# Kernel tuning notes

Measured on AMD Instinct MI355X. Metric: run time of the kernel, lower is better.

Reference implementation:

```python
import jax, jax.numpy as jnp
import numpy as np

N, E, G = 50000, 320000, 256
BN_EPS = 1e-5
HEADS = 4


def _bn(x, g, b):
    # eval-mode BatchNorm1d with running_mean=0, running_var=1
    return g * (x * np.float32(1.0 / np.sqrt(1.0 + BN_EPS))) + b


def _mlp(x, w1, b1, w2, b2):
    return jax.nn.relu(x @ w1 + b1) @ w2 + b2


def _gatv2(x, src, dst, ea, lw, lb, rw, rb, ew, att, bias):
    n = x.shape[0]
    H = HEADS
    C = lw.shape[1] // H
    # self-loops with edge_attr = mean of incoming edge features (fill_value='mean')
    deg = jax.ops.segment_sum(jnp.ones((ea.shape[0],), x.dtype), dst, num_segments=n)
    loop_ea = jax.ops.segment_sum(ea, dst, num_segments=n) / jnp.maximum(deg, 1.0)[:, None]
    ar = jnp.arange(n)
    s = jnp.concatenate([src, ar])
    d = jnp.concatenate([dst, ar])
    ea_all = jnp.concatenate([ea, loop_ea], axis=0)
    xl = (x @ lw + lb).reshape(n, H, C)   # lin_l (source / message features)
    xr = (x @ rw + rb).reshape(n, H, C)   # lin_r (target)
    ee = (ea_all @ ew).reshape(-1, H, C)  # lin_edge (no bias)
    m = jax.nn.leaky_relu(xl[s] + xr[d] + ee, 0.2)       # [E+N, H, C]
    a = jnp.einsum('ehc,hc->eh', m, att)                 # attention logits
    amax = jax.ops.segment_max(a, d, num_segments=n)
    ex = jnp.exp(a - amax[d])
    den = jax.ops.segment_sum(ex, d, num_segments=n)
    w = ex / den[d]                                      # scatter-softmax over target
    out = jax.ops.segment_sum(xl[s] * w[..., None], d, num_segments=n)
    return out.reshape(n, H * C) + bias


def _meta(x, ea, u, src, dst, batch, ep, gp, up):
    # EdgeModel -> NodeModel(GATv2 + relu) -> GlobalModel (residuals=False, eval dropout)
    ea2 = _mlp(jnp.concatenate([x[src], x[dst], ea], axis=1), *ep)
    xn = jax.nn.relu(_gatv2(x, src, dst, ea2, *gp))
    pooled = jax.ops.segment_sum(xn, batch, num_segments=G)
    u2 = _mlp(jnp.concatenate([u, pooled], axis=1), *up)
    return xn, ea2, u2


def _forward(x, edge_attr, e1_w1, e1_b1, e1_w2, e1_b2, g1_lw, g1_lb, g1_rw, g1_rb, g1_ew, g1_att, g1_bias, u1_w1, u1_b1, u1_w2, u1_b2, bn_n_g, bn_n_b, bn_e_g, bn_e_b, bn_u_g, bn_u_b, e2_w1, e2_b1, e2_w2, e2_b2, g2_lw, g2_lb, g2_rw, g2_rb, g2_ew, g2_att, g2_bias, u2_w1, u2_b1, u2_w2, u2_b2, fc1_w, fc1_b, fc2_w, fc2_b, src, dst, batch):
    u0 = jnp.zeros((G, 256), x.dtype)
    x1, ea1, u1 = _meta(x, edge_attr, u0, src, dst, batch,
                        (e1_w1, e1_b1, e1_w2, e1_b2),
                        (g1_lw, g1_lb, g1_rw, g1_rb, g1_ew, g1_att, g1_bias),
                        (u1_w1, u1_b1, u1_w2, u1_b2))
    x1 = _bn(x1, bn_n_g, bn_n_b)
    ea1 = _bn(ea1, bn_e_g, bn_e_b)
    u1 = _bn(u1, bn_u_g, bn_u_b)
    _, _, u2 = _meta(x1, ea1, u1, src, dst, batch,
                     (e2_w1, e2_b1, e2_w2, e2_b2),
                     (g2_lw, g2_lb, g2_rw, g2_rb, g2_ew, g2_att, g2_bias),
                     (u2_w1, u2_b1, u2_w2, u2_b2))
    h = jax.nn.relu(u2 @ fc1_w + fc1_b)
    return h @ fc2_w + fc2_b


def setup_inputs() -> dict:
    key = jax.random.key(0)
    ks = iter(jax.random.split(key, 64))
    rp = lambda shape: jax.random.normal(next(ks), shape, jnp.float32) * 0.05
    inp = {}
    inp['x'] = jax.random.normal(next(ks), (N, 64), jnp.float32)
    inp['edge_attr'] = jax.random.normal(next(ks), (E, 16), jnp.float32)
    # layer 1: EdgeModel(64,16,h=64,out=128), GATv2(64->256,H=4,edge=128), Global(256+256->256)
    inp.update(e1_w1=rp((144, 64)), e1_b1=rp((64,)), e1_w2=rp((64, 128)), e1_b2=rp((128,)))
    inp.update(g1_lw=rp((64, 256)), g1_lb=rp((256,)), g1_rw=rp((64, 256)), g1_rb=rp((256,)),
               g1_ew=rp((128, 256)), g1_att=rp((4, 64)), g1_bias=rp((256,)))
    inp.update(u1_w1=rp((512, 256)), u1_b1=rp((256,)), u1_w2=rp((256, 256)), u1_b2=rp((256,)))
    inp.update(bn_n_g=jnp.ones((256,), jnp.float32), bn_n_b=jnp.zeros((256,), jnp.float32),
               bn_e_g=jnp.ones((128,), jnp.float32), bn_e_b=jnp.zeros((128,), jnp.float32),
               bn_u_g=jnp.ones((256,), jnp.float32), bn_u_b=jnp.zeros((256,), jnp.float32))
    # layer 2: EdgeModel(256,128,h=128,out=128), GATv2(256->256,H=4,edge=128), Global
    inp.update(e2_w1=rp((640, 128)), e2_b1=rp((128,)), e2_w2=rp((128, 128)), e2_b2=rp((128,)))
    inp.update(g2_lw=rp((256, 256)), g2_lb=rp((256,)), g2_rw=rp((256, 256)), g2_rb=rp((256,)),
               g2_ew=rp((128, 256)), g2_att=rp((4, 64)), g2_bias=rp((256,)))
    inp.update(u2_w1=rp((512, 256)), u2_b1=rp((256,)), u2_w2=rp((256, 256)), u2_b2=rp((256,)))
    inp.update(fc1_w=rp((256, 64)), fc1_b=rp((64,)), fc2_w=rp((64, 1)), fc2_b=rp((1,)))
    inp['edge_index'] = jax.random.randint(next(ks), (2, E), 0, N, jnp.int64)
    inp['batch'] = jnp.sort(jax.random.randint(next(ks), (N,), 0, G, jnp.int64))
    return inp


def reference(x, edge_attr, e1_w1, e1_b1, e1_w2, e1_b2, g1_lw, g1_lb, g1_rw, g1_rb, g1_ew, g1_att, g1_bias, u1_w1, u1_b1, u1_w2, u1_b2, bn_n_g, bn_n_b, bn_e_g, bn_e_b, bn_u_g, bn_u_b, e2_w1, e2_b1, e2_w2, e2_b2, g2_lw, g2_lb, g2_rw, g2_rb, g2_ew, g2_att, g2_bias, u2_w1, u2_b1, u2_w2, u2_b2, fc1_w, fc1_b, fc2_w, fc2_b, edge_index, batch):
    return _forward(x, edge_attr, e1_w1, e1_b1, e1_w2, e1_b2, g1_lw, g1_lb, g1_rw, g1_rb, g1_ew, g1_att, g1_bias, u1_w1, u1_b1, u1_w2, u1_b2, bn_n_g, bn_n_b, bn_e_g, bn_e_b, bn_u_g, bn_u_b, e2_w1, e2_b1, e2_w2, e2_b2, g2_lw, g2_lb, g2_rw, g2_rb, g2_ew, g2_att, g2_bias, u2_w1, u2_b1, u2_w2, u2_b2, fc1_w, fc1_b, fc2_w, fc2_b, edge_index[0], edge_index[1], batch)
```

## Files before the change

### kernel.cpp

```cpp
#include <hip/hip_runtime.h>
#include <hip/hip_bf16.h>
#include <hip/hip_fp8.h>
#include <cstdint>
#include <cstddef>

#define INVS 0.99999500003749968f
#define G_GRAPHS 256

using bf16 = __hip_bfloat16;
using short8 = __attribute__((ext_vector_type(8))) short;
using floatx4 = __attribute__((ext_vector_type(4))) float;

__device__ __forceinline__ unsigned short f2bf(float v) {
    union { float f; unsigned u; } x; x.f = v;
    unsigned r = x.u + 0x7fffu + ((x.u >> 16) & 1u);
    return (unsigned short)(r >> 16);
}
__device__ __forceinline__ float bfu(unsigned short u) { return __uint_as_float((unsigned)u << 16); }
__device__ __forceinline__ unsigned char f2fp8(float v) {
    __hip_fp8_e4m3 q(v); return q.__x;
}
__device__ __forceinline__ float fp82f(unsigned char b) {
    __hip_fp8_e4m3 q; q.__x = b; return (float)q;
}

__global__ void degi_k(const int* __restrict__ dst, int* __restrict__ degi, int E) {
    int gid = blockIdx.x * 256 + threadIdx.x;
    if (gid < E) atomicAdd(&degi[dst[gid]], 1);
}

__global__ __launch_bounds__(1024) void scan_blk_k(const int* __restrict__ degi,
                                                   int* __restrict__ off,
                                                   int* __restrict__ bsum, int N) {
    __shared__ int buf[1024];
    int t = threadIdx.x;
    int base = blockIdx.x * 2048;
    int i0 = base + 2 * t, i1 = base + 2 * t + 1;
    int v0 = (i0 < N) ? (degi[i0] + 1) : 0;
    int v1 = (i1 < N) ? (degi[i1] + 1) : 0;
    int s = v0 + v1;
    buf[t] = s;
    __syncthreads();
    for (int ofs = 1; ofs < 1024; ofs <<= 1) {
        int add = (t >= ofs) ? buf[t - ofs] : 0;
        __syncthreads();
        buf[t] += add;
        __syncthreads();
    }
    int excl = buf[t] - s;
    if (i0 < N) off[i0] = excl;
    if (i1 < N) off[i1] = excl + v0;
    if (t == 1023) bsum[blockIdx.x] = buf[1023];
}

__global__ void scan_top_k(const int* __restrict__ bsum, int* __restrict__ boff,
                           int* __restrict__ off, int NBLK, int N) {
    if (threadIdx.x == 0 && blockIdx.x == 0) {
        int run = 0;
        for (int i = 0; i < NBLK; ++i) { boff[i] = run; run += bsum[i]; }
        off[N] = run;
    }
}

__global__ void scan_add_k(int* __restrict__ off, const int* __restrict__ boff, int N) {
    int gid = blockIdx.x * 256 + threadIdx.x;
    if (gid < N) off[gid] += boff[gid >> 11];
}

__global__ void fill_csr_k(const int* __restrict__ src, const int* __restrict__ dst,
                           const int* __restrict__ off, int* __restrict__ fillc,
                           int* __restrict__ csr_src, int* __restrict__ csr_dst,
                           int* __restrict__ csr_eid, int E, int N) {
    int gid = blockIdx.x * 256 + threadIdx.x;
    if (gid < E) {
        int d = dst[gid];
        int slot = off[d] + atomicAdd(&fillc[d], 1);
        csr_src[slot] = src[gid];
        csr_dst[slot] = d;
        csr_eid[slot] = gid;
    }
    if (gid < N) {
        int slot = off[gid + 1] - 1;
        csr_src[slot] = gid;
        csr_dst[slot] = gid;
        csr_eid[slot] = E + gid;
    }
}

__global__ void conv_weights1_k(const float* __restrict__ w1, const float* __restrict__ w2,
                                short* __restrict__ w1p, short* __restrict__ w1c,
                                short* __restrict__ w2s) {
    int gid = blockIdx.x * 256 + threadIdx.x;
    if (gid < 1024) {
        int f = gid >> 6, lane = gid & 63;
        int kk = f >> 3, tt = f & 7;
        int n = tt * 16 + (lane & 15);
        int k0 = kk * 32 + (lane >> 4) * 8;
        short8 v;
        for (int j = 0; j < 8; ++j) {
            int k = k0 + j;
            float x = (n < 64) ? w1[k * 64 + n] : w1[(64 + k) * 64 + (n - 64)];
            v[j] = (short)f2bf(x);
        }
        *(short8*)(w1p + (long long)gid * 8) = v;
    } else if (gid < 1280) {
        int g2 = gid - 1024;
        int tt = g2 >> 6, lane = g2 & 63;
        int n = tt * 16 + (lane & 15);
        int k0 = (lane >> 4) * 8;
        short8 v;
        for (int j = 0; j < 8; ++j) {
            int k = k0 + j;
            v[j] = (k < 16) ? (short)f2bf(w1[(128 + k) * 64 + n]) : (short)0;
        }
        *(short8*)(w1c + (long long)g2 * 8) = v;
    } else if (gid < 2304) {
        int g2 = gid - 1280;
        int f = g2 >> 6, lane = g2 & 63;
        int kk = f >> 3, tt = f & 7;
        int n = tt * 16 + (lane & 15);
        int k0 = kk * 32 + (lane >> 4) * 8;
        short8 v;
        for (int j = 0; j < 8; ++j) v[j] = (short)f2bf(w2[(k0 + j) * 128 + n]);
        *(short8*)(w2s + (long long)g2 * 8) = v;
    }
}

__global__ void conv_ew_k(const float* __restrict__ ew, short* __restrict__ ews) {
    int gid = blockIdx.x * 256 + threadIdx.x;
    if (gid >= 4096) return;
    int f = gid >> 6, lane = gid & 63;
    int kk = f >> 4, tt = f & 15;
    int n = tt * 16 + (lane & 15);
    int k0 = kk * 32 + (lane >> 4) * 8;
    short8 v;
    for (int j = 0; j < 8; ++j) v[j] = (short)f2bf(ew[(k0 + j) * 256 + n]);
    *(short8*)(ews + (long long)gid * 8) = v;
}

template <int K>
__global__ void conv_nodew_k(const float* __restrict__ wl, const float* __restrict__ wr,
                             short* __restrict__ out) {
    int gid = blockIdx.x * 256 + threadIdx.x;
    if (gid >= (K / 32) * 32 * 64) return;
    int f = gid >> 6, lane = gid & 63;
    int kk = f >> 5, tt = f & 31;
    int n = tt * 16 + (lane & 15);
    int k0 = kk * 32 + (lane >> 4) * 8;
    short8 v;
    for (int j = 0; j < 8; ++j) {
        int k = k0 + j;
        float x = (n < 256) ? wl[k * 256 + n] : wr[k * 256 + (n - 256)];
        v[j] = (short)f2bf(x);
    }
    *(short8*)(out + (long long)gid * 8) = v;
}

__global__ void conv_pre2w_k(const float* __restrict__ w1, short* __restrict__ out) {
    int gid = blockIdx.x * 256 + threadIdx.x;
    if (gid >= 8 * 16 * 64) return;
    int f = gid >> 6, lane = gid & 63;
    int kk = f >> 4, tt = f & 15;
    int n = tt * 16 + (lane & 15);
    int k0 = kk * 32 + (lane >> 4) * 8;
    short8 v;
    for (int j = 0; j < 8; ++j) {
        int k = k0 + j;
        float x = (n < 128) ? w1[k * 128 + n] : w1[(256 + k) * 128 + (n - 128)];
        v[j] = (short)f2bf(x);
    }
    *(short8*)(out + (long long)gid * 8) = v;
}

__global__ __launch_bounds__(256) void pre1_mfma_k(
    const float* __restrict__ x, const short* __restrict__ w1p,
    const float* __restrict__ b1, bf16* __restrict__ pre1, int N) {
    __shared__ short At[16][72];
    __shared__ short Ot[16][136];
    int t = threadIdx.x;
    long long n0 = (long long)blockIdx.x * 16;
    {
        int r = t >> 4, c = t & 15;
        long long n = n0 + r;
        float4 v = {0.f, 0.f, 0.f, 0.f};
        if (n < N) v = *(const float4*)(x + n * 64 + c * 4);
        ushort4 pk;
        pk.x = f2bf(v.x); pk.y = f2bf(v.y); pk.z = f2bf(v.z); pk.w = f2bf(v.w);
        *(ushort4*)&At[r][c * 4] = pk;
    }
    __syncthreads();
    int w = t >> 6, lane = t & 63;
    int nq = w * 2;
    int lr = lane & 15, lq = lane >> 4;
    floatx4 acc[2];
    for (int i = 0; i < 2; ++i) acc[i] = (floatx4){0.f, 0.f, 0.f, 0.f};
    for (int kk = 0; kk < 2; ++kk) {
        short8 a = *(const short8*)&At[lr][kk * 32 + lq * 8];
        for (int tt = 0; tt < 2; ++tt) {
            short8 b = *(const short8*)(w1p + ((long long)((kk * 8 + nq + tt) * 64 + lane)) * 8);
            acc[tt] = __builtin_amdgcn_mfma_f32_16x16x32_bf16(a, b, acc[tt], 0, 0, 0);
        }
    }
    for (int tt = 0; tt < 2; ++tt) {
        int col = (nq + tt) * 16 + lr;
        float bv = (col >= 64) ? b1[col - 64] : 0.f;
        for (int r = 0; r < 4; ++r)
            Ot[lq * 4 + r][col] = (short)f2bf(acc[tt][r] + bv);
    }
    __syncthreads();
    {
        int r = t >> 4, c = t & 15;
        long long n = n0 + r;
        if (n < N)
            *(short8*)(void*)(pre1 + n * 128 + c * 8) = *(const short8*)&Ot[r][c * 8];
    }
}

__global__ __launch_bounds__(256) void edge_mlp1_mfma_k(
    const bf16* __restrict__ pre1, const float* __restrict__ ea,
    const int* __restrict__ csr_src, const int* __restrict__ csr_dst,
    const int* __restrict__ csr_eid,
    const short* __restrict__ w1c,
    const short* __restrict__ w2s, const float* __restrict__ b2,
    const short* __restrict__ ews,
    bf16* __restrict__ out, unsigned char* __restrict__ ee8, int NT, int E) {
    __shared__ float Ps[32][68];
    __shared__ short Ae[32][40];
    __shared__ short Ht[32][72];
    __shared__ short A2[32][136];
    __shared__ int sdv[32][3];
    unsigned char* Et = (unsigned char*)&Ps[0][0];
    int t = threadIdx.x;
    long long s0 = (long long)blockIdx.x * 32;
    if (t < 96) {
        int r = t & 31, which = t >> 5;
        long long s = s0 + r;
        int v = (which == 2) ? E : 0;
        if (s < NT) v = (which == 0) ? csr_src[s] : (which == 1 ? csr_dst[s] : csr_eid[s]);
        sdv[r][which] = v;
    }
    __syncthreads();
    {
        int r = t >> 3, c = t & 7;
        long long s = s0 + r;
        bool ok = (s < NT) && (sdv[r][2] < E);
        float p[8];
        if (ok) {
            short8 vs = *(const short8*)(const void*)(pre1 + (long long)sdv[r][0] * 128 + c * 8);
            short8 vd = *(const short8*)(const void*)(pre1 + (long long)sdv[r][1] * 128 + 64 + c * 8);
            for (int j = 0; j < 8; ++j)
                p[j] = bfu((unsigned short)vs[j]) + bfu((unsigned short)vd[j]);
        } else {
            for (int j = 0; j < 8; ++j) p[j] = 0.f;
        }
        for (int j = 0; j < 8; ++j) Ps[r][c * 8 + j] = p[j];
    }
    if (t < 128) {
        int r = t >> 2, c = t & 3;
        long long s = s0 + r;
        int eid = sdv[r][2];
        float4 v = {0.f, 0.f, 0.f, 0.f};
        if (s < NT && eid < E) v = *(const float4*)(ea + (long long)eid * 16 + c * 4);
        ushort4 pk;
        pk.x = f2bf(v.x); pk.y = f2bf(v.y); pk.z = f2bf(v.z); pk.w = f2bf(v.w);
        *(ushort4*)&Ae[r][c * 4] = pk;
    } else {
        int i = t - 128;
        int r = i >> 2, c = i & 3;
        *(ushort4*)&Ae[r][16 + c * 4] = (ushort4){0, 0, 0, 0};
    }
    __syncthreads();

    int w = t >> 6, lane = t & 63;
    int m0 = (w & 1) * 16;
    int lr = lane & 15, lq = lane >> 4;

    {
        int nq1 = (w >> 1) * 2;
        floatx4 acc[2];
        for (int tt = 0; tt < 2; ++tt) {
            int col = (nq1 + tt) * 16 + lr;
            for (int r = 0; r < 4; ++r) acc[tt][r] = Ps[m0 + lq * 4 + r][col];
        }
        short8 a = *(const short8*)&Ae[m0 + lr][lq * 8];
        for (int tt = 0; tt < 2; ++tt) {
            short8 b = *(const short8*)(w1c + ((long long)((nq1 + tt) * 64 + lane)) * 8);
            acc[tt] = __builtin_amdgcn_mfma_f32_16x16x32_bf16(a, b, acc[tt], 0, 0, 0);
        }
        for (int tt = 0; tt < 2; ++tt) {
            int col = (nq1 + tt) * 16 + lr;
            for (int r = 0; r < 4; ++r)
                Ht[m0 + lq * 4 + r][col] = (short)f2bf(fmaxf(acc[tt][r], 0.f));
        }
    }
    __syncthreads();

    {
        int nq2 = (w >> 1) * 4;
        floatx4 acc2[4];
        for (int i = 0; i < 4; ++i) acc2[i] = (floatx4){0.f, 0.f, 0.f, 0.f};
        for (int kk = 0; kk < 2; ++kk) {
            short8 a = *(const short8*)&Ht[m0 + lr][kk * 32 + lq * 8];
            for (int tt = 0; tt < 4; ++tt) {
                short8 b = *(const short8*)(w2s + ((long long)((kk * 8 + nq2 + tt) * 64 + lane)) * 8);
                acc2[tt] = __builtin_amdgcn_mfma_f32_16x16x32_bf16(a, b, acc2[tt], 0, 0, 0);
            }
        }
        for (int tt = 0; tt < 4; ++tt) {
            int col = (nq2 + tt) * 16 + lr;
            float bv = b2[col];
            for (int r = 0; r < 4; ++r)
                A2[m0 + lq * 4 + r][col] = (short)f2bf(acc2[tt][r] + bv);
        }
    }
    __syncthreads();

    {
        int nq3 = (w >> 1) * 8;
        floatx4 acc3[8];
        for (int i = 0; i < 8; ++i) acc3[i] = (floatx4){0.f, 0.f, 0.f, 0.f};
        for (int kk = 0; kk < 4; ++kk) {
            short8 a = *(const short8*)&A2[m0 + lr][kk * 32 + lq * 8];
            for (int tt = 0; tt < 8; ++tt) {
                short8 b = *(const short8*)(ews + ((long long)((kk * 16 + nq3 + tt) * 64 + lane)) * 8);
                acc3[tt] = __builtin_amdgcn_mfma_f32_16x16x32_bf16(a, b, acc3[tt], 0, 0, 0);
            }
        }
        for (int tt = 0; tt < 8; ++tt) {
            int col = (nq3 + tt) * 16 + lr;
            for (int r = 0; r < 4; ++r)
                Et[(m0 + lq * 4 + r) * 272 + col] = f2fp8(acc3[tt][r]);
        }
    }
    for (int i = t; i < 512; i += 256) {
        int r = i >> 4, c = i & 15;
        long long s = s0 + r;
        if (s < NT)
            *(short8*)(void*)(out + s * 128 + c * 8) = *(const short8*)&A2[r][c * 8];
    }
    __syncthreads();
    for (int i = t; i < 512; i += 256) {
        int r = i >> 4, c = i & 15;
        long long s = s0 + r;
        if (s < NT)
            *(uint4*)(ee8 + s * 256 + c * 16) = *(const uint4*)(Et + r * 272 + c * 16);
    }
}

template <int K, typename T>
__global__ __launch_bounds__(256) void node_linear_mfma_k(
    const T* x, const short* __restrict__ ws,
    const float* __restrict__ bl, const float* __restrict__ br,
    bf16* __restrict__ xl, bf16* xr, int N) {
    __shared__ short At[16][K + 8];
    __shared__ short Ot[16][520];
    int t = threadIdx.x;
    long long n0 = (long long)blockIdx.x * 16;
    if (sizeof(T) == 4) {
        for (int i = t; i < 16 * (K / 4); i += 256) {
            int r = i / (K / 4), c = i % (K / 4);
            long long n = n0 + r;
            float4 v = {0.f, 0.f, 0.f, 0.f};
            if (n < N) v = *(const float4*)((const float*)x + n * K + c * 4);
            ushort4 pk;
            pk.x = f2bf(v.x); pk.y = f2bf(v.y); pk.z = f2bf(v.z); pk.w = f2bf(v.w);
            *(ushort4*)&At[r][c * 4] = pk;
        }
    } else {
        for (int i = t; i < 16 * (K / 8); i += 256) {
            int r = i / (K / 8), c = i % (K / 8);
            long long n = n0 + r;
            short8 v = {0, 0, 0, 0, 0, 0, 0, 0};
            if (n < N) v = *(const short8*)(const void*)((const bf16*)x + n * K + c * 8);
            *(short8*)&At[r][c * 8] = v;
        }
    }
    __syncthreads();

    int w = t >> 6, lane = t & 63;
    int nq = w * 8;
    int lr = lane & 15, lq = lane >> 4;

    floatx4 acc[8];
    for (int i = 0; i < 8; ++i) acc[i] = (floatx4){0.f, 0.f, 0.f, 0.f};
    for (int kk = 0; kk < K / 32; ++kk) {
        short8 a = *(const short8*)&At[lr][kk * 32 + lq * 8];
        for (int tt = 0; tt < 8; ++tt) {
            short8 b = *(const short8*)(ws + ((long long)((kk * 32 + nq + tt) * 64 + lane)) * 8);
            acc[tt] = __builtin_amdgcn_mfma_f32_16x16x32_bf16(a, b, acc[tt], 0, 0, 0);
        }
    }
    for (int tt = 0; tt < 8; ++tt) {
        int col = (nq + tt) * 16 + lr;
        float bv = (col < 256) ? bl[col] : br[col - 256];
        for (int r = 0; r < 4; ++r)
            Ot[lq * 4 + r][col] = (short)f2bf(acc[tt][r] + bv);
    }
    __syncthreads();
    for (int i = t; i < 1024; i += 256) {
        int r = i >> 6, c = i & 63;
        long long n = n0 + r;
        if (n < N) {
            short8 v = *(const short8*)&Ot[r][c * 8];
            if (c < 32) *(short8*)(void*)(xl + n * 256 + c * 8) = v;
            else        *(short8*)(void*)(xr + n * 256 + (c - 32) * 8) = v;
        }
    }
}

__global__ __launch_bounds__(256) void pre_mfma_k(
    const bf16* __restrict__ x, const short* __restrict__ ws,
    const float* __restrict__ bx, bf16* __restrict__ out, int N) {
    __shared__ short At[16][264];
    __shared__ short Ot[16][264];
    int t = threadIdx.x;
    long long n0 = (long long)blockIdx.x * 16;
    for (int i = t; i < 512; i += 256) {
        int r = i >> 5, c = i & 31;
        long long n = n0 + r;
        short8 v = {0, 0, 0, 0, 0, 0, 0, 0};
        if (n < N) v = *(const short8*)(const void*)(x + n * 256 + c * 8);
        *(short8*)&At[r][c * 8] = v;
    }
    __syncthreads();

    int w = t >> 6, lane = t & 63;
    int nq = w * 4;
    int lr = lane & 15, lq = lane >> 4;

    floatx4 acc[4];
    for (int i = 0; i < 4; ++i) acc[i] = (floatx4){0.f, 0.f, 0.f, 0.f};
    for (int kk = 0; kk < 8; ++kk) {
        short8 a = *(const short8*)&At[lr][kk * 32 + lq * 8];
        for (int tt = 0; tt < 4; ++tt) {
            short8 b = *(const short8*)(ws + ((long long)((kk * 16 + nq + tt) * 64 + lane)) * 8);
            acc[tt] = __builtin_amdgcn_mfma_f32_16x16x32_bf16(a, b, acc[tt], 0, 0, 0);
        }
    }
    for (int tt = 0; tt < 4; ++tt) {
        int col = (nq + tt) * 16 + lr;
        float bv = bx[col];
        for (int r = 0; r < 4; ++r)
            Ot[lq * 4 + r][col] = (short)f2bf(acc[tt][r] + bv);
    }
    __syncthreads();
    for (int i = t; i < 512; i += 256) {
        int r = i >> 5, c = i & 31;
        long long n = n0 + r;
        if (n < N)
            *(short8*)(void*)(out + n * 256 + c * 8) = *(const short8*)&Ot[r][c * 8];
    }
}

template <bool L1>
__global__ __launch_bounds__(256) void gat_fused_k(
    const unsigned char* __restrict__ ee8, const bf16* __restrict__ xl, const bf16* xr,
    const int* __restrict__ off, const int* __restrict__ csr_src,
    const float* __restrict__ att, const float* __restrict__ bias,
    const float* __restrict__ bng, const float* __restrict__ bnb,
    const int* __restrict__ batch,
    bf16* x1bn, float* __restrict__ pooled, int N) {
    __shared__ float ps[4][260];
    __shared__ int bid[4];
    int t = threadIdx.x;
    int w = t >> 6, lane = t & 63;
    int n = blockIdx.x * 4 + w;
    bool valid = n < N;
    int c0 = lane * 4;
    float o0 = 0.f, o1 = 0.f, o2 = 0.f, o3 = 0.f;
    if (valid) {
        ushort4 xrp = *(const ushort4*)(const void*)(xr + (long long)n * 256 + c0);
        ushort4 xop = *(const ushort4*)(const void*)(xl + (long long)n * 256 + c0);
        float xr0 = bfu(xrp.x), xr1 = bfu(xrp.y), xr2 = bfu(xrp.z), xr3 = bfu(xrp.w);
        float4 atv = *(const float4*)(att + c0);
        float a0 = 0.f, a1 = 0.f, a2 = 0.f, a3 = 0.f, dacc = 0.f;
        float es0 = 0.f, es1 = 0.f, es2 = 0.f, es3 = 0.f;
        int beg = off[n], end1 = off[n + 1] - 1;
        ushort4 xlp;
        unsigned ep;
        {
            int sid = csr_src[beg];
            xlp = *(const ushort4*)(const void*)(xl + (long long)sid * 256 + c0);
            ep = *(const unsigned*)(ee8 + (long long)beg * 256 + c0);
        }
        for (int i = beg; i < end1; ++i) {
            ushort4 cx = xlp;
            unsigned ce = ep;
            if (i + 1 < end1) {
                int sid = csr_src[i + 1];
                xlp = *(const ushort4*)(const void*)(xl + (long long)sid * 256 + c0);
                ep = *(const unsigned*)(ee8 + (long long)(i + 1) * 256 + c0);
            }
            float x0 = bfu(cx.x), x1 = bfu(cx.y), x2 = bfu(cx.z), x3 = bfu(cx.w);
            float e0 = fp82f(ce & 0xff);
            float e1 = fp82f((ce >> 8) & 0xff);
            float e2 = fp82f((ce >> 16) & 0xff);
            float e3 = fp82f(ce >> 24);
            es0 += e0; es1 += e1; es2 += e2; es3 += e3;
            float m0 = x0 + xr0 + e0;
            float m1 = x1 + xr1 + e1;
            float m2 = x2 + xr2 + e2;
            float m3 = x3 + xr3 + e3;
            m0 = m0 > 0.f ? m0 : 0.2f * m0;
            m1 = m1 > 0.f ? m1 : 0.2f * m1;
            m2 = m2 > 0.f ? m2 : 0.2f * m2;
            m3 = m3 > 0.f ? m3 : 0.2f * m3;
            float p = atv.x * m0 + atv.y * m1 + atv.z * m2 + atv.w * m3;
            p += __shfl_xor(p, 1, 64);
            p += __shfl_xor(p, 2, 64);
            p += __shfl_xor(p, 4, 64);
            p += __shfl_xor(p, 8, 64);
            float ex = expf(p);
            a0 += ex * x0; a1 += ex * x1; a2 += ex * x2; a3 += ex * x3;
            dacc += ex;
        }
        {
            float rdv = 1.f / fmaxf((float)(end1 - beg), 1.f);
            float x0 = bfu(xop.x), x1 = bfu(xop.y), x2 = bfu(xop.z), x3 = bfu(xop.w);
            float m0 = x0 + xr0 + es0 * rdv;
            float m1 = x1 + xr1 + es1 * rdv;
            float m2 = x2 + xr2 + es2 * rdv;
            float m3 = x3 + xr3 + es3 * rdv;
            m0 = m0 > 0.f ? m0 : 0.2f * m0;
            m1 = m1 > 0.f ? m1 : 0.2f * m1;
            m2 = m2 > 0.f ? m2 : 0.2f * m2;
            m3 = m3 > 0.f ? m3 : 0.2f * m3;
            float p = atv.x * m0 + atv.y * m1 + atv.z * m2 + atv.w * m3;
            p += __shfl_xor(p, 1, 64);
            p += __shfl_xor(p, 2, 64);
            p += __shfl_xor(p, 4, 64);
            p += __shfl_xor(p, 8, 64);
            float ex = expf(p);
            a0 += ex * x0; a1 += ex * x1; a2 += ex * x2; a3 += ex * x3;
            dacc += ex;
        }
        float inv = 1.f / dacc;
        o0 = fmaxf(a0 * inv + bias[c0],     0.f);
        o1 = fmaxf(a1 * inv + bias[c0 + 1], 0.f);
        o2 = fmaxf(a2 * inv + bias[c0 + 2], 0.f);
        o3 = fmaxf(a3 * inv + bias[c0 + 3], 0.f);
        if (L1) {
            ushort4 o;
            o.x = f2bf(bng[c0]     * (o0 * INVS) + bnb[c0]);
            o.y = f2bf(bng[c0 + 1] * (o1 * INVS) + bnb[c0 + 1]);
            o.z = f2bf(bng[c0 + 2] * (o2 * INVS) + bnb[c0 + 2]);
            o.w = f2bf(bng[c0 + 3] * (o3 * INVS) + bnb[c0 + 3]);
            *(ushort4*)(void*)(x1bn + (long long)n * 256 + c0) = o;
        }
    }
    if (lane == 0) bid[w] = valid ? batch[n] : -1;
    ps[w][c0]     = o0;
    ps[w][c0 + 1] = o1;
    ps[w][c0 + 2] = o2;
    ps[w][c0 + 3] = o3;
    __syncthreads();
    int b0 = bid[0];
    bool same = (b0 >= 0)
             && (bid[1] < 0 || bid[1] == b0)
             && (bid[2] < 0 || bid[2] == b0)
             && (bid[3] < 0 || bid[3] == b0);
    if (same) {
        float s = ps[0][t] + ps[1][t] + ps[2][t] + ps[3][t];
        atomicAdd(&pooled[(long long)b0 * 256 + t], s);
    } else if (valid) {
        long long pb = (long long)bid[w] * 256 + c0;
        atomicAdd(&pooled[pb],     o0);
        atomicAdd(&pooled[pb + 1], o1);
        atomicAdd(&pooled[pb + 2], o2);
        atomicAdd(&pooled[pb + 3], o3);
    }
}

__global__ void global_mlp1_k(const float* __restrict__ pooled,
                              const float* __restrict__ w1, const float* __restrict__ b1,
                              const float* __restrict__ w2, const float* __restrict__ b2,
                              const float* __restrict__ bng, const float* __restrict__ bnb,
                              float* __restrict__ u1bn) {
    __shared__ float pr[256];
    __shared__ float h[256];
    int t = threadIdx.x, g = blockIdx.x;
    pr[t] = pooled[g * 256 + t];
    __syncthreads();
    float acc = b1[t];
    for (int k = 0; k < 256; ++k) acc += pr[k] * w1[(256 + k) * 256 + t];
    h[t] = fmaxf(acc, 0.f);
    __syncthreads();
    float a2 = b2[t];
    for (int k = 0; k < 256; ++k) a2 += h[k] * w2[k * 256 + t];
    u1bn[g * 256 + t] = bng[t] * (a2 * INVS) + bnb[t];
}

__global__ void conv_weights_k(const float* __restrict__ w1, const float* __restrict__ w2,
                               const float* __restrict__ b1,
                               const float* __restrict__ bg, const float* __restrict__ bb,
                               short* __restrict__ w1s, short* __restrict__ w2s,
                               float* __restrict__ b1x) {
    int gid = blockIdx.x * 256 + threadIdx.x;
    if (gid < 10240) {
        int f = gid >> 6, lane = gid & 63;
        int kk = f >> 3, tt = f & 7;
        int n = tt * 16 + (lane & 15);
        int k0 = kk * 32 + (lane >> 4) * 8;
        short8 v;
        for (int j = 0; j < 8; ++j) {
            int k = k0 + j;
            float x = w1[k * 128 + n];
            if (k >= 512) x *= bg[k - 512] * INVS;
            v[j] = (short)f2bf(x);
        }
        *(short8*)(w1s + (long long)gid * 8) = v;
    } else if (gid < 12288) {
        int g2 = gid - 10240;
        int f = g2 >> 6, lane = g2 & 63;
        int kk = f >> 3, tt = f & 7;
        int n = tt * 16 + (lane & 15);
        int k0 = kk * 32 + (lane >> 4) * 8;
        short8 v;
        for (int j = 0; j < 8; ++j) v[j] = (short)f2bf(w2[(k0 + j) * 128 + n]);
        *(short8*)(w2s + (long long)g2 * 8) = v;
    } else if (gid < 12544) {
        int j = gid - 12288;
        b1x[j] = 0.f;
    } else if (gid < 12672) {
        int j = gid - 12544;
        float acc = b1[j];
        for (int c = 0; c < 128; ++c) acc += bb[c] * w1[(512 + c) * 128 + j];
        b1x[128 + j] = acc;
    }
}

__global__ __launch_bounds__(256) void edge_mlp2_mfma_k(
    const bf16* __restrict__ xpre, const bf16* __restrict__ ea_slot,
    const int* __restrict__ csr_src, const int* __restrict__ csr_dst,
    const int* __restrict__ csr_eid,
    const short* __restrict__ w1s,
    const short* __restrict__ w2s, const float* __restrict__ b2,
    const short* __restrict__ ews,
    unsigned char* __restrict__ ee8, int NT, int E) {
    __shared__ float Ps[32][132];
    __shared__ short At[32][136];
    __shared__ short Ht[32][136];
    __shared__ int sdv[32][3];
    unsigned char* Et = (unsigned char*)&Ps[0][0];
    int t = threadIdx.x;
    long long s0 = (long long)blockIdx.x * 32;
    if (t < 96) {
        int r = t & 31, which = t >> 5;
        long long s = s0 + r;
        int v = (which == 2) ? E : 0;
        if (s < NT) v = (which == 0) ? csr_src[s] : (which == 1 ? csr_dst[s] : csr_eid[s]);
        sdv[r][which] = v;
    }
    __syncthreads();
    for (int i = t; i < 512; i += 256) {
        int r = i >> 4, c = i & 15;
        long long s = s0 + r;
        bool ok = (s < NT) && (sdv[r][2] < E);
        float p[8];
        if (ok) {
            short8 vs = *(const short8*)(const void*)(xpre + (long long)sdv[r][0] * 256 + c * 8);
            short8 vd = *(const short8*)(const void*)(xpre + (long long)sdv[r][1] * 256 + 128 + c * 8);
            for (int j = 0; j < 8; ++j)
                p[j] = bfu((unsigned short)vs[j]) + bfu((unsigned short)vd[j]);
        } else {
            for (int j = 0; j < 8; ++j) p[j] = 0.f;
        }
        for (int j = 0; j < 8; ++j) Ps[r][c * 8 + j] = p[j];
    }
    for (int i = t; i < 512; i += 256) {
        int r = i >> 4, c = i & 15;
        long long s = s0 + r;
        short8 v = {0, 0, 0, 0, 0, 0, 0, 0};
        if (s < NT && sdv[r][2] < E)
            v = *(const short8*)(const void*)(ea_slot + s * 128 + c * 8);
        *(short8*)&At[r][c * 8] = v;
    }
    __syncthreads();

    int w = t >> 6, lane = t & 63;
    int m0 = (w & 1) * 16;
    int nq = (w >> 1) * 4;
    int lr = lane & 15, lq = lane >> 4;

    floatx4 acc[4];
    for (int tt = 0; tt < 4; ++tt) {
        int col = (nq + tt) * 16 + lr;
        for (int r = 0; r < 4; ++r) acc[tt][r] = Ps[m0 + lq * 4 + r][col];
    }
    for (int kk = 0; kk < 4; ++kk) {
        short8 a = *(const short8*)&At[m0 + lr][kk * 32 + lq * 8];
        for (int tt = 0; tt < 4; ++tt) {
            short8 b = *(const short8*)(w1s + ((long long)(((16 + kk) * 8 + nq + tt) * 64 + lane)) * 8);
            acc[tt] = __builtin_amdgcn_mfma_f32_16x16x32_bf16(a, b, acc[tt], 0, 0, 0);
        }
    }
    for (int tt = 0; tt < 4; ++tt) {
        int col = (nq + tt) * 16 + lr;
        for (int r = 0; r < 4; ++r)
            Ht[m0 + lq * 4 + r][col] = (short)f2bf(fmaxf(acc[tt][r], 0.f));
    }
    __syncthreads();

    floatx4 acc2[4];
    for (int i = 0; i < 4; ++i) acc2[i] = (floatx4){0.f, 0.f, 0.f, 0.f};
    for (int kk = 0; kk < 4; ++kk) {
        short8 a = *(const short8*)&Ht[m0 + lr][kk * 32 + lq * 8];
        for (int tt = 0; tt < 4; ++tt) {
            short8 b = *(const short8*)(w2s + ((long long)((kk * 8 + nq + tt) * 64 + lane)) * 8);
            acc2[tt] = __builtin_amdgcn_mfma_f32_16x16x32_bf16(a, b, acc2[tt], 0, 0, 0);
        }
    }
    for (int tt = 0; tt < 4; ++tt) {
        int col = (nq + tt) * 16 + lr;
        float bv = b2[col];
        for (int r = 0; r < 4; ++r)
            At[m0 + lq * 4 + r][col] = (short)f2bf(acc2[tt][r] + bv);
    }
    __syncthreads();
    {
        int nq3 = (w >> 1) * 8;
        floatx4 acc3[8];
        for (int i = 0; i < 8; ++i) acc3[i] = (floatx4){0.f, 0.f, 0.f, 0.f};
        for (int kk = 0; kk < 4; ++kk) {
            short8 a = *(const short8*)&At[m0 + lr][kk * 32 + lq * 8];
            for (int tt = 0; tt < 8; ++tt) {
                short8 b = *(const short8*)(ews + ((long long)((kk * 16 + nq3 + tt) * 64 + lane)) * 8);
                acc3[tt] = __builtin_amdgcn_mfma_f32_16x16x32_bf16(a, b, acc3[tt], 0, 0, 0);
            }
        }
        for (int tt = 0; tt < 8; ++tt) {
            int col = (nq3 + tt) * 16 + lr;
            for (int r = 0; r < 4; ++r)
                Et[(m0 + lq * 4 + r) * 272 + col] = f2fp8(acc3[tt][r]);
        }
    }
    __syncthreads();
    for (int i = t; i < 512; i += 256) {
        int r = i >> 4, c = i & 15;
        long long s = s0 + r;
        if (s < NT && sdv[r][2] < E)
            *(uint4*)(ee8 + s * 256 + c * 16) = *(const uint4*)(Et + r * 272 + c * 16);
    }
}

__global__ void final_mlp_k(const float* __restrict__ u1bn, const float* __restrict__ pooled,
                            const float* __restrict__ w1, const float* __restrict__ b1,
                            const float* __restrict__ w2, const float* __restrict__ b2,
                            const float* __restrict__ f1w, const float* __restrict__ f1b,
                            const float* __restrict__ f2w, const float* __restrict__ f2b,
                            float* __restrict__ out) {
    __shared__ float ub[256], pb[256], h[256], u2[256];
    int t = threadIdx.x, g = blockIdx.x;
    ub[t] = u1bn[g * 256 + t];
    pb[t] = pooled[g * 256 + t];
    __syncthreads();
    float acc = b1[t];
    for (int k = 0; k < 256; ++k)
        acc += ub[k] * w1[k * 256 + t] + pb[k] * w1[(256 + k) * 256 + t];
    h[t] = fmaxf(acc, 0.f);
    __syncthreads();
    float a2 = b2[t];
    for (int k = 0; k < 256; ++k) a2 += h[k] * w2[k * 256 + t];
    u2[t] = a2;
    __syncthreads();
    float fv = 0.f;
    if (t < 64) {
        float a3 = f1b[t];
        for (int k = 0; k < 256; ++k) a3 += u2[k] * f1w[k * 64 + t];
        fv = fmaxf(a3, 0.f) * f2w[t];
    }
    for (int off = 32; off; off >>= 1) fv += __shfl_down(fv, off, 64);
    if (t == 0) out[g] = fv + f2b[0];
}

extern "C" void kernel_launch(void* const* d_in, const int* in_sizes, int n_in,
                              void* d_out, int out_size, void* d_ws, size_t ws_size,
                              hipStream_t stream) {
    const float* x         = (const float*)d_in[0];
    const float* edge_attr = (const float*)d_in[1];
    const float* e1_w1 = (const float*)d_in[2];
    const float* e1_b1 = (const float*)d_in[3];
    const float* e1_w2 = (const float*)d_in[4];
    const float* e1_b2 = (const float*)d_in[5];
    const float* g1_lw = (const float*)d_in[6];
    const float* g1_lb = (const float*)d_in[7];
    const float* g1_rw = (const float*)d_in[8];
    const float* g1_rb = (const float*)d_in[9];
    const float* g1_ew = (const float*)d_in[10];
    const float* g1_att = (const float*)d_in[11];
    const float* g1_bias = (const float*)d_in[12];
    const float* u1_w1 = (const float*)d_in[13];
    const float* u1_b1 = (const float*)d_in[14];
    const float* u1_w2 = (const float*)d_in[15];
    const float* u1_b2 = (const float*)d_in[16];
    const float* bn_n_g = (const float*)d_in[17];
    const float* bn_n_b = (const float*)d_in[18];
    const float* bn_e_g = (const float*)d_in[19];
    const float* bn_e_b = (const float*)d_in[20];
    const float* bn_u_g = (const float*)d_in[21];
    const float* bn_u_b = (const float*)d_in[22];
    const float* e2_w1 = (const float*)d_in[23];
    const float* e2_b1 = (const float*)d_in[24];
    const float* e2_w2 = (const float*)d_in[25];
    const float* e2_b2 = (const float*)d_in[26];
    const float* g2_lw = (const float*)d_in[27];
    const float* g2_lb = (const float*)d_in[28];
    const float* g2_rw = (const float*)d_in[29];
    const float* g2_rb = (const float*)d_in[30];
    const float* g2_ew = (const float*)d_in[31];
    const float* g2_att = (const float*)d_in[32];
    const float* g2_bias = (const float*)d_in[33];
    const float* u2_w1 = (const float*)d_in[34];
    const float* u2_b1 = (const float*)d_in[35];
    const float* u2_w2 = (const float*)d_in[36];
    const float* u2_b2 = (const float*)d_in[37];
    const float* fc1_w = (const float*)d_in[38];
    const float* fc1_b = (const float*)d_in[39];
    const float* fc2_w = (const float*)d_in[40];
    const float* fc2_b = (const float*)d_in[41];
    const int* edge_index = (const int*)d_in[42];
    const int* batch = (const int*)d_in[43];

    const int N = in_sizes[0] / 64;
    const int E = in_sizes[1] / 16;
    const int NT = E + N;
    const int G = G_GRAPHS;
    const int* src = edge_index;
    const int* dst = edge_index + E;
    const int NB = (NT + 31) / 32;
    const int NSB = (N + 2047) / 2048;

    char* p = (char*)d_ws;
    auto alloc = [&](size_t bytes) { char* r = p; p += (bytes + 255) & ~(size_t)255; return r; };
    bf16* eabuf = (bf16*)alloc((size_t)NT * 128 * 2);
    bf16* xl    = (bf16*)alloc((size_t)N * 256 * 2);
    bf16* xr    = (bf16*)alloc((size_t)N * 256 * 2);
    bf16* x1bn  = xr;
    unsigned char* ee8 = (unsigned char*)alloc((size_t)NT * 256);
    bf16* pre1  = (bf16*)alloc((size_t)N * 128 * 2);
    int* degi   = (int*)alloc((size_t)N * 4);
    int* off    = (int*)alloc((size_t)(N + 1) * 4);
    int* fillc  = (int*)alloc((size_t)N * 4);
    int* csr_src = (int*)alloc((size_t)NT * 4);
    int* csr_dst = (int*)alloc((size_t)NT * 4);
    int* csr_eid = (int*)alloc((size_t)NT * 4);
    int* bsum   = (int*)alloc((size_t)(NSB + 1) * 4);
    int* boff   = (int*)alloc((size_t)(NSB + 1) * 4);
    float* pooled = (float*)alloc((size_t)G * 256 * 4);
    float* u1bn = (float*)alloc((size_t)G * 256 * 4);
    short* w1s  = (short*)alloc((size_t)20 * 8 * 64 * 8 * 2);
    short* w2s  = (short*)alloc((size_t)4 * 8 * 64 * 8 * 2);
    float* b1x  = (float*)alloc((size_t)256 * 4);
    short* w1p  = (short*)alloc((size_t)16 * 64 * 8 * 2);
    short* w1c  = (short*)alloc((size_t)4 * 64 * 8 * 2);
    short* w2s1 = (short*)alloc((size_t)16 * 64 * 8 * 2);
    short* ews1 = (short*)alloc((size_t)4 * 16 * 64 * 8 * 2);
    short* ews2 = (short*)alloc((size_t)4 * 16 * 64 * 8 * 2);
    short* nw1  = (short*)alloc((size_t)2 * 32 * 64 * 8 * 2);
    short* nw2  = (short*)alloc((size_t)8 * 32 * 64 * 8 * 2);
    short* nwp  = (short*)alloc((size_t)8 * 16 * 64 * 8 * 2);

    hipMemsetAsync(degi, 0, (size_t)N * 4, stream);
    hipMemsetAsync(fillc, 0, (size_t)N * 4, stream);
    hipMemsetAsync(pooled, 0, (size_t)G * 256 * 4, stream);
    degi_k<<<(E + 255) / 256, 256, 0, stream>>>(dst, degi, E);
    scan_blk_k<<<NSB, 1024, 0, stream>>>(degi, off, bsum, N);
    scan_top_k<<<1, 64, 0, stream>>>(bsum, boff, off, NSB, N);
    scan_add_k<<<(N + 255) / 256, 256, 0, stream>>>(off, boff, N);
    fill_csr_k<<<(max(E, N) + 255) / 256, 256, 0, stream>>>(src, dst, off, fillc,
                                                            csr_src, csr_dst, csr_eid, E, N);

    conv_weights1_k<<<9, 256, 0, stream>>>(e1_w1, e1_w2, w1p, w1c, w2s1);
    conv_ew_k<<<16, 256, 0, stream>>>(g1_ew, ews1);
    conv_ew_k<<<16, 256, 0, stream>>>(g2_ew, ews2);
    conv_nodew_k<64><<<16, 256, 0, stream>>>(g1_lw, g1_rw, nw1);
    conv_nodew_k<256><<<64, 256, 0, stream>>>(g2_lw, g2_rw, nw2);
    conv_pre2w_k<<<32, 256, 0, stream>>>(e2_w1, nwp);
    pre1_mfma_k<<<(N + 15) / 16, 256, 0, stream>>>(x, w1p, e1_b1, pre1, N);
    edge_mlp1_mfma_k<<<NB, 256, 0, stream>>>(pre1, edge_attr, csr_src, csr_dst, csr_eid,
                                             w1c, w2s1, e1_b2, ews1, eabuf, ee8, NT, E);
    node_linear_mfma_k<64, float><<<(N + 15) / 16, 256, 0, stream>>>(x, nw1, g1_lb, g1_rb, xl, xr, N);
    gat_fused_k<true><<<(N + 3) / 4, 256, 0, stream>>>(ee8, xl, xr, off, csr_src,
                                                       g1_att, g1_bias, bn_n_g, bn_n_b,
                                                       batch, x1bn, pooled, N);
    global_mlp1_k<<<G, 256, 0, stream>>>(pooled, u1_w1, u1_b1, u1_w2, u1_b2, bn_u_g, bn_u_b, u1bn);

    conv_weights_k<<<50, 256, 0, stream>>>(e2_w1, e2_w2, e2_b1, bn_e_g, bn_e_b, w1s, w2s, b1x);
    pre_mfma_k<<<(N + 15) / 16, 256, 0, stream>>>(x1bn, nwp, b1x, xl, N);
    edge_mlp2_mfma_k<<<NB, 256, 0, stream>>>(xl, eabuf, csr_src, csr_dst, csr_eid,
                                             w1s, w2s, e2_b2, ews2, ee8, NT, E);
    node_linear_mfma_k<256, bf16><<<(N + 15) / 16, 256, 0, stream>>>(x1bn, nw2, g2_lb, g2_rb, xl, xr, N);
    hipMemsetAsync(pooled, 0, (size_t)G * 256 * 4, stream);
    gat_fused_k<false><<<(N + 3) / 4, 256, 0, stream>>>(ee8, xl, xr, off, csr_src,
                                                        g2_att, g2_bias, nullptr, nullptr,
                                                        batch, nullptr, pooled, N);
    final_mlp_k<<<G, 256, 0, stream>>>(u1bn, pooled, u2_w1, u2_b1, u2_w2, u2_b2,
                                       fc1_w, fc1_b, fc2_w, fc2_b, (float*)d_out);
}
```

Baseline: 826.5 us.

## Recompute layer-1 edge features inside edge_mlp2 instead of storing them

Stops edge_mlp1 from writing its bf16 edge-feature output (NT x 128) to global memory. edge_mlp2 now recomputes those features itself from pre1 gathers, the raw edge_attr and the layer-1 MLP weights. This trades one write and one read of roughly 95 MB of edge data for extra gathers of pre1 rows and two small MFMA stages in the second edge kernel. It also removes the eabuf workspace allocation.

```diff
diff --git a/kernel.cpp b/kernel.cpp
--- a/kernel.cpp
+++ b/kernel.cpp
@@ -223,7 +223,7 @@
     const short* __restrict__ w1c,
     const short* __restrict__ w2s, const float* __restrict__ b2,
     const short* __restrict__ ews,
-    bf16* __restrict__ out, unsigned char* __restrict__ ee8, int NT, int E) {
+    unsigned char* __restrict__ ee8, int NT, int E) {
     __shared__ float Ps[32][68];
     __shared__ short Ae[32][40];
     __shared__ short Ht[32][72];
@@ -331,12 +331,6 @@
             for (int r = 0; r < 4; ++r)
                 Et[(m0 + lq * 4 + r) * 272 + col] = f2fp8(acc3[tt][r]);
         }
-    }
-    for (int i = t; i < 512; i += 256) {
-        int r = i >> 4, c = i & 15;
-        long long s = s0 + r;
-        if (s < NT)
-            *(short8*)(void*)(out + s * 128 + c * 8) = *(const short8*)&A2[r][c * 8];
     }
     __syncthreads();
     for (int i = t; i < 512; i += 256) {
@@ -630,9 +624,12 @@
 }
 
 __global__ __launch_bounds__(256) void edge_mlp2_mfma_k(
-    const bf16* __restrict__ xpre, const bf16* __restrict__ ea_slot,
+    const bf16* __restrict__ xpre, const bf16* __restrict__ pre1,
+    const float* __restrict__ ea,
     const int* __restrict__ csr_src, const int* __restrict__ csr_dst,
     const int* __restrict__ csr_eid,
+    const short* __restrict__ w1c, const short* __restrict__ w2s1,
+    const float* __restrict__ e1_b2,
     const short* __restrict__ w1s,
     const short* __restrict__ w2s, const float* __restrict__ b2,
     const short* __restrict__ ews,
@@ -640,6 +637,7 @@
     __shared__ float Ps[32][132];
     __shared__ short At[32][136];
     __shared__ short Ht[32][136];
+    __shared__ short Ae[32][40];
     __shared__ int sdv[32][3];
     unsigned char* Et = (unsigned char*)&Ps[0][0];
     int t = threadIdx.x;
@@ -652,6 +650,62 @@
         sdv[r][which] = v;
     }
     __syncthreads();
+    {
+        int r = t >> 3, c = t & 7;
+        long long s = s0 + r;
+        bool ok = (s < NT) && (sdv[r][2] < E);
+        float p[8];
+        if (ok) {
+            short8 vs = *(const short8*)(const void*)(pre1 + (long long)sdv[r][0] * 128 + c * 8);
+            short8 vd = *(const short8*)(const void*)(pre1 + (long long)sdv[r][1] * 128 + 64 + c * 8);
+            for (int j = 0; j < 8; ++j)
+                p[j] = bfu((unsigned short)vs[j]) + bfu((unsigned short)vd[j]);
+        } else {
+            for (int j = 0; j < 8; ++j) p[j] = 0.f;
+        }
+        for (int j = 0; j < 8; ++j) Ps[r][c * 8 + j] = p[j];
+    }
+    if (t < 128) {
+        int r = t >> 2, c = t & 3;
+        long long s = s0 + r;
+        int eid = sdv[r][2];
+        float4 v = {0.f, 0.f, 0.f, 0.f};
+        if (s < NT && eid < E) v = *(const float4*)(ea + (long long)eid * 16 + c * 4);
+        ushort4 pk;
+        pk.x = f2bf(v.x); pk.y = f2bf(v.y); pk.z = f2bf(v.z); pk.w = f2bf(v.w);
+        *(ushort4*)&Ae[r][c * 4] = pk;
+    } else {
+        int i = t - 128;
+        int r = i >> 2, c = i & 3;
+        *(ushort4*)&Ae[r][16 + c * 4] = (ushort4){0, 0, 0, 0};
+    }
+    __syncthreads();
+
+    int w = t >> 6, lane = t & 63;
+    int m0 = (w & 1) * 16;
+    int nq = (w >> 1) * 4;
+    int lr = lane & 15, lq = lane >> 4;
+
+    {
+        int nq1 = (w >> 1) * 2;
+        floatx4 acc[2];
+        for (int tt = 0; tt < 2; ++tt) {
+            int col = (nq1 + tt) * 16 + lr;
+            for (int r = 0; r < 4; ++r) acc[tt][r] = Ps[m0 + lq * 4 + r][col];
+        }
+        short8 a = *(const short8*)&Ae[m0 + lr][lq * 8];
+        for (int tt = 0; tt < 2; ++tt) {
+            short8 b = *(const short8*)(w1c + ((long long)((nq1 + tt) * 64 + lane)) * 8);
+            acc[tt] = __builtin_amdgcn_mfma_f32_16x16x32_bf16(a, b, acc[tt], 0, 0, 0);
+        }
+        for (int tt = 0; tt < 2; ++tt) {
+            int col = (nq1 + tt) * 16 + lr;
+            for (int r = 0; r < 4; ++r)
+                Ht[m0 + lq * 4 + r][col] = (short)f2bf(fmaxf(acc[tt][r], 0.f));
+        }
+    }
+    __syncthreads();
+
     for (int i = t; i < 512; i += 256) {
         int r = i >> 4, c = i & 15;
         long long s = s0 + r;
@@ -667,20 +721,24 @@
         }
         for (int j = 0; j < 8; ++j) Ps[r][c * 8 + j] = p[j];
     }
-    for (int i = t; i < 512; i += 256) {
-        int r = i >> 4, c = i & 15;
-        long long s = s0 + r;
-        short8 v = {0, 0, 0, 0, 0, 0, 0, 0};
-        if (s < NT && sdv[r][2] < E)
-            v = *(const short8*)(const void*)(ea_slot + s * 128 + c * 8);
-        *(short8*)&At[r][c * 8] = v;
-    }
-    __syncthreads();
-
-    int w = t >> 6, lane = t & 63;
-    int m0 = (w & 1) * 16;
-    int nq = (w >> 1) * 4;
-    int lr = lane & 15, lq = lane >> 4;
+    {
+        floatx4 acc2[4];
+        for (int i = 0; i < 4; ++i) acc2[i] = (floatx4){0.f, 0.f, 0.f, 0.f};
+        for (int kk = 0; kk < 2; ++kk) {
+            short8 a = *(const short8*)&Ht[m0 + lr][kk * 32 + lq * 8];
+            for (int tt = 0; tt < 4; ++tt) {
+                short8 b = *(const short8*)(w2s1 + ((long long)((kk * 8 + nq + tt) * 64 + lane)) * 8);
+                acc2[tt] = __builtin_amdgcn_mfma_f32_16x16x32_bf16(a, b, acc2[tt], 0, 0, 0);
+            }
+        }
+        for (int tt = 0; tt < 4; ++tt) {
+            int col = (nq + tt) * 16 + lr;
+            float bv = e1_b2[col];
+            for (int r = 0; r < 4; ++r)
+                At[m0 + lq * 4 + r][col] = (short)f2bf(acc2[tt][r] + bv);
+        }
+    }
+    __syncthreads();
 
     floatx4 acc[4];
     for (int tt = 0; tt < 4; ++tt) {
@@ -832,7 +890,6 @@
 
     char* p = (char*)d_ws;
     auto alloc = [&](size_t bytes) { char* r = p; p += (bytes + 255) & ~(size_t)255; return r; };
-    bf16* eabuf = (bf16*)alloc((size_t)NT * 128 * 2);
     bf16* xl    = (bf16*)alloc((size_t)N * 256 * 2);
     bf16* xr    = (bf16*)alloc((size_t)N * 256 * 2);
     bf16* x1bn  = xr;
@@ -878,7 +935,7 @@
     conv_pre2w_k<<<32, 256, 0, stream>>>(e2_w1, nwp);
     pre1_mfma_k<<<(N + 15) / 16, 256, 0, stream>>>(x, w1p, e1_b1, pre1, N);
     edge_mlp1_mfma_k<<<NB, 256, 0, stream>>>(pre1, edge_attr, csr_src, csr_dst, csr_eid,
-                                             w1c, w2s1, e1_b2, ews1, eabuf, ee8, NT, E);
+                                             w1c, w2s1, e1_b2, ews1, ee8, NT, E);
     node_linear_mfma_k<64, float><<<(N + 15) / 16, 256, 0, stream>>>(x, nw1, g1_lb, g1_rb, xl, xr, N);
     gat_fused_k<true><<<(N + 3) / 4, 256, 0, stream>>>(ee8, xl, xr, off, csr_src,
                                                        g1_att, g1_bias, bn_n_g, bn_n_b,
@@ -887,8 +944,9 @@
 
     conv_weights_k<<<50, 256, 0, stream>>>(e2_w1, e2_w2, e2_b1, bn_e_g, bn_e_b, w1s, w2s, b1x);
     pre_mfma_k<<<(N + 15) / 16, 256, 0, stream>>>(x1bn, nwp, b1x, xl, N);
-    edge_mlp2_mfma_k<<<NB, 256, 0, stream>>>(xl, eabuf, csr_src, csr_dst, csr_eid,
-                                             w1s, w2s, e2_b2, ews2, ee8, NT, E);
+    edge_mlp2_mfma_k<<<NB, 256, 0, stream>>>(xl, pre1, edge_attr, csr_src, csr_dst, csr_eid,
+                                             w1c, w2s1, e1_b2, w1s, w2s, e2_b2, ews2,
+                                             ee8, NT, E);
     node_linear_mfma_k<256, bf16><<<(N + 15) / 16, 256, 0, stream>>>(x1bn, nw2, g2_lb, g2_rb, xl, xr, N);
     hipMemsetAsync(pooled, 0, (size_t)G * 256 * 4, stream);
     gat_fused_k<false><<<(N + 3) / 4, 256, 0, stream>>>(ee8, xl, xr, off, csr_src,
```

Result: faster. 778.1 us (-5.8%).
